# Kernel tuning notes

Measured on AMD Instinct MI355X. Metric: run time of the kernel, lower is better.

## Reference

```python
import jax, jax.numpy as jnp
import numpy as np

I3 = jnp.eye(3, dtype=jnp.float32)
G_VEC = jnp.array([0.0, 0.0, -9.80665], dtype=jnp.float32)
# Q diag: [cov_omega x3, cov_acc x3, cov_b_omega x3, cov_b_acc x3, cov_Rot_c_i x3, cov_t_c_i x3]
Q_DIAG = jnp.array([1e-3] * 3 + [1e-2] * 3 + [6e-9] * 3 + [2e-4] * 3 + [1e-9] * 3 + [1e-9] * 3, dtype=jnp.float32)
N_NORM_ROT = 100
N_NORM_ROT_CI = 1000


def skew(v):
    z = jnp.zeros_like(v[0])
    return jnp.stack([jnp.stack([z, -v[2], v[1]]),
                      jnp.stack([v[2], z, -v[0]]),
                      jnp.stack([-v[1], v[0], z])])


def so3exp(phi):
    a2 = jnp.sum(phi * phi)
    small = a2 < 1e-12
    a = jnp.sqrt(jnp.where(small, 1.0, a2))
    axis = phi / a
    c, s = jnp.cos(a), jnp.sin(a)
    big = c * I3 + (1.0 - c) * jnp.outer(axis, axis) + s * skew(axis)
    return jnp.where(small, I3 + skew(phi), big)


def sen3exp(xi):
    # SE_2(3) exponential: xi[:3]=rotation, xi[3:9]=(v, p) parts
    phi = xi[:3]
    a2 = jnp.sum(phi * phi)
    small = a2 < 1e-12
    a = jnp.sqrt(jnp.where(small, 1.0, a2))
    axis = phi / a
    c, s = jnp.cos(a), jnp.sin(a)
    sk = skew(axis)
    R = jnp.where(small, I3 + skew(phi),
                  c * I3 + (1.0 - c) * jnp.outer(axis, axis) + s * sk)
    J = jnp.where(small, I3 + 0.5 * skew(phi),
                  (s / a) * I3 + (1.0 - s / a) * jnp.outer(axis, axis) + ((1.0 - c) / a) * sk)
    x = J @ xi[3:].reshape(2, 3).T  # (3,2): columns are dv, dp
    return R, x


def normalize_rot(R):
    # Polar-factor re-orthonormalization (equivalent to the SVD-based
    # normalize_rot for near-rotation matrices), via Newton-Schulz iteration
    # which is smooth and jit/vjp friendly.
    def body(X, _):
        return 1.5 * X - 0.5 * (X @ X.T @ X), None
    X, _ = jax.lax.scan(body, R, None, length=8)
    return X


def from_rpy(roll, pitch, yaw):
    cr, sr = jnp.cos(roll), jnp.sin(roll)
    cp, sp = jnp.cos(pitch), jnp.sin(pitch)
    cy, sy = jnp.cos(yaw), jnp.sin(yaw)
    one = jnp.ones_like(cr)
    zero = jnp.zeros_like(cr)
    Rx = jnp.stack([jnp.stack([one, zero, zero]), jnp.stack([zero, cr, -sr]), jnp.stack([zero, sr, cr])])
    Ry = jnp.stack([jnp.stack([cp, zero, sp]), jnp.stack([zero, one, zero]), jnp.stack([-sp, zero, cp])])
    Rz = jnp.stack([jnp.stack([cy, -sy, zero]), jnp.stack([sy, cy, zero]), jnp.stack([zero, zero, one])])
    return Rz @ Ry @ Rx


def init_covariance():
    P = jnp.zeros((21, 21), dtype=jnp.float32)
    P = P.at[:2, :2].set(1e-3 * jnp.eye(2))     # cov_Rot0 (no yaw error)
    P = P.at[3:5, 3:5].set(0.1 * jnp.eye(2))    # cov_v0
    P = P.at[9:12, 9:12].set(6e-3 * I3)         # cov_b_omega0
    P = P.at[12:15, 12:15].set(4e-3 * I3)       # cov_b_acc0
    P = P.at[15:18, 15:18].set(1e-6 * I3)       # cov_Rot_c_i0
    P = P.at[18:21, 18:21].set(5e-3 * I3)       # cov_t_c_i0
    return P


def propagate_cov(P, Rot, v, p, dt):
    F = jnp.zeros((21, 21), dtype=P.dtype)
    F = F.at[3:6, :3].set(skew(G_VEC))
    F = F.at[6:9, 3:6].set(I3)
    F = F.at[:3, 9:12].set(-Rot)
    F = F.at[3:6, 9:12].set(-skew(v) @ Rot)
    F = F.at[3:6, 12:15].set(-Rot)
    F = F.at[6:9, 9:12].set(-skew(p) @ Rot)
    G = jnp.zeros((21, 18), dtype=P.dtype)
    G = G.at[:3, :3].set(Rot)
    G = G.at[3:6, 3:6].set(Rot)
    G = G.at[9:12, 6:9].set(I3)
    G = G.at[12:15, 9:12].set(I3)
    G = G.at[15:18, 12:15].set(I3)
    G = G.at[18:21, 15:18].set(I3)
    F = F * dt
    G = G * dt
    F2 = F @ F
    Phi = jnp.eye(21, dtype=P.dtype) + F + 0.5 * F2 + (F2 @ F) / 6.0  # 3rd-order expm
    return Phi @ (P + (G * Q_DIAG[None, :]) @ G.T) @ Phi.T


def _step(carry, xs):
    Rot, v, p, b_om, b_ac, Rci, tci, P = carry
    u_i, dt_i, mcov_i, i = xs
    # ---- propagate ----
    acc = Rot @ (u_i[3:6] - b_ac) + G_VEC
    v_n = v + acc * dt_i
    p_n = p + v * dt_i + 0.5 * acc * dt_i * dt_i
    Rot_n = Rot @ so3exp((u_i[:3] - b_om) * dt_i)
    P_n = propagate_cov(P, Rot, v, p, dt_i)
    # ---- update: zero lateral/vertical body-velocity pseudo-measurement ----
    omega = u_i[:3] - b_om
    Rot_body = Rot_n @ Rci
    v_imu = Rot_n.T @ v_n
    v_body = Rci.T @ v_imu + skew(tci) @ omega
    H = jnp.zeros((2, 21), dtype=P.dtype)
    H = H.at[:, 3:6].set(Rot_body.T[1:])
    H = H.at[:, 15:18].set((Rci.T @ skew(v_imu))[1:])
    H = H.at[:, 9:12].set(skew(tci)[1:])
    H = H.at[:, 18:21].set(-skew(omega)[1:])
    r = -v_body[1:]
    Rm = jnp.diag(mcov_i)
    S = H @ P_n @ H.T + Rm                    # (2,2)
    K = jnp.linalg.solve(S, H @ P_n).T        # K = P H^T S^-1 (P, S symmetric)
    dx = K @ r                                 # (21,)
    dR, dxi = sen3exp(dx[:9])
    Rot_u = dR @ Rot_n
    v_u = dR @ v_n + dxi[:, 0]
    p_u = dR @ p_n + dxi[:, 1]
    b_om_u = b_om + dx[9:12]
    b_ac_u = b_ac + dx[12:15]
    Rci_u = so3exp(dx[15:18]) @ Rci
    tci_u = tci + dx[18:21]
    IKH = jnp.eye(21, dtype=P.dtype) - K @ H
    P_u = IKH @ P_n @ IKH.T + K @ Rm @ K.T    # Joseph form
    P_u = 0.5 * (P_u + P_u.T)
    Rot_u = jnp.where(i % N_NORM_ROT == 0, normalize_rot(Rot_u), Rot_u)
    Rci_u = jnp.where(i % N_NORM_ROT_CI == 0, normalize_rot(Rci_u), Rci_u)
    carry = (Rot_u, v_u, p_u, b_om_u, b_ac_u, Rci_u, tci_u, P_u)
    return carry, (Rot_u, v_u, p_u, b_om_u, b_ac_u, Rci_u, tci_u)


def _forward(t, u, measurements_covs, v_mes, p_mes, ang0, N):
    dt = t[1:N] - t[:N - 1]
    Rot0 = from_rpy(ang0[0], ang0[1], ang0[2])
    z3 = jnp.zeros(3, dtype=u.dtype)
    carry0 = (Rot0, v_mes[0], z3, z3, z3, I3, z3, init_covariance())
    xs = (u[1:N], dt, measurements_covs[1:N], jnp.arange(1, N))
    _, ys = jax.lax.scan(_step, carry0, xs)
    Rot = jnp.concatenate([Rot0[None], ys[0]], axis=0)
    v = jnp.concatenate([v_mes[0][None], ys[1]], axis=0)
    p = jnp.concatenate([z3[None], ys[2]], axis=0)
    b_omega = jnp.concatenate([z3[None], ys[3]], axis=0)
    b_acc = jnp.concatenate([z3[None], ys[4]], axis=0)
    Rot_c_i = jnp.concatenate([I3[None], ys[5]], axis=0)
    t_c_i = jnp.concatenate([z3[None], ys[6]], axis=0)
    return (Rot, v, p, b_omega, b_acc, Rot_c_i, t_c_i)


def setup_inputs() -> dict:
    key = jax.random.key(0)
    N = 20000  # 200 s at 100 Hz IMU
    k0, k1, k2, k3, k4, k5 = jax.random.split(key, 6)
    t = jnp.arange(N, dtype=jnp.float32) * 0.01
    gyro = 0.01 * jax.random.normal(k0, (N, 3), dtype=jnp.float32)
    acc = jnp.array([0.0, 0.0, 9.80665], jnp.float32) + 0.1 * jax.random.normal(k1, (N, 3), dtype=jnp.float32)
    u = jnp.concatenate([gyro, acc], axis=1)
    measurements_covs = 0.1 + jax.random.uniform(k2, (N, 2), dtype=jnp.float32)
    v_mes = jax.random.normal(k3, (N, 3), dtype=jnp.float32)
    p_mes = jax.random.normal(k4, (N, 3), dtype=jnp.float32)
    ang0 = 0.01 * jax.random.normal(k5, (3,), dtype=jnp.float32)
    return dict(t=t, u=u, measurements_covs=measurements_covs, v_mes=v_mes, p_mes=p_mes, ang0=ang0, N=N)


def reference(t, u, measurements_covs, v_mes, p_mes, ang0, N):
    return _forward(t, u, measurements_covs, v_mes, p_mes, ang0, N)
```

## Files before the change

kernel.cpp:

```cpp
#include <hip/hip_runtime.h>

#define GRAV 9.80665f
#define WAVE_SYNC() do { \
    asm volatile("s_waitcnt lgkmcnt(0)" ::: "memory"); \
    __builtin_amdgcn_sched_barrier(0); \
  } while(0)

#define LDP 28

__device__ __forceinline__ float sel3(int r, float a0, float a1, float a2){
  float x = (r==1)? a1 : a0;
  return (r>=2)? a2 : x;
}
__device__ __forceinline__ float RL(float v, int k){
  return __int_as_float(__builtin_amdgcn_readlane(__float_as_int(v), k));
}
__device__ __forceinline__ float pick9(int k, const float* X){
  float s=X[0];
  s=(k==1)?X[1]:s; s=(k==2)?X[2]:s; s=(k==3)?X[3]:s; s=(k==4)?X[4]:s;
  s=(k==5)?X[5]:s; s=(k==6)?X[6]:s; s=(k==7)?X[7]:s; s=(k==8)?X[8]:s;
  return s;
}

__device__ __forceinline__ void mm33(float* __restrict__ O, const float* A, const float* B){
#pragma unroll
  for(int r=0;r<3;++r){
#pragma unroll
    for(int c=0;c<3;++c){
      O[r*3+c] = A[r*3+0]*B[0*3+c] + A[r*3+1]*B[1*3+c] + A[r*3+2]*B[2*3+c];
    }
  }
}

__device__ __forceinline__ void rot_from_t2(float t_, float p0, float p1, float p2, float* R){
  float c_, k1_, k2_;
  if (t_ < 1e-4f){
    c_  = 1.f - t_*(0.5f - t_*((1.f/24.f) - t_*(1.f/720.f)));
    k2_ = 1.f - t_*((1.f/6.f) - t_*((1.f/120.f) - t_*(1.f/5040.f)));
    k1_ = 0.5f - t_*((1.f/24.f) - t_*(1.f/720.f));
  } else {
    float a = sqrtf(t_);
    c_ = __cosf(a);
    float s = __sinf(a);
    k2_ = s/a;
    k1_ = (1.f - c_)/t_;
  }
  R[0]=c_+k1_*p0*p0;      R[1]=k1_*p0*p1-k2_*p2;  R[2]=k1_*p0*p2+k2_*p1;
  R[3]=k1_*p0*p1+k2_*p2;  R[4]=c_+k1_*p1*p1;      R[5]=k1_*p1*p2-k2_*p0;
  R[6]=k1_*p0*p2-k2_*p1;  R[7]=k1_*p1*p2+k2_*p0;  R[8]=c_+k1_*p2*p2;
}

__device__ __forceinline__ void normalize_rot9(float* X){
#pragma unroll 1
  for(int it=0; it<8; ++it){
    float Y[9], Z[9];
#pragma unroll
    for(int r=0;r<3;++r)
#pragma unroll
      for(int c=0;c<3;++c)
        Y[r*3+c] = X[r*3+0]*X[c*3+0] + X[r*3+1]*X[c*3+1] + X[r*3+2]*X[c*3+2];
#pragma unroll
    for(int r=0;r<3;++r)
#pragma unroll
      for(int c=0;c<3;++c)
        Z[r*3+c] = Y[r*3+0]*X[0*3+c] + Y[r*3+1]*X[1*3+c] + Y[r*3+2]*X[2*3+c];
#pragma unroll
    for(int e=0;e<9;++e) X[e] = 1.5f*X[e] - 0.5f*Z[e];
  }
}

__device__ __forceinline__ float pick_state(int l,
    const float* Rt, const float* vv, const float* pp,
    const float* bw, const float* ba, const float* Rc, const float* tc){
  float s = Rt[0];
  s=(l==1)?Rt[1]:s;  s=(l==2)?Rt[2]:s;  s=(l==3)?Rt[3]:s;  s=(l==4)?Rt[4]:s;
  s=(l==5)?Rt[5]:s;  s=(l==6)?Rt[6]:s;  s=(l==7)?Rt[7]:s;  s=(l==8)?Rt[8]:s;
  s=(l==9)?vv[0]:s;  s=(l==10)?vv[1]:s; s=(l==11)?vv[2]:s;
  s=(l==12)?pp[0]:s; s=(l==13)?pp[1]:s; s=(l==14)?pp[2]:s;
  s=(l==15)?bw[0]:s; s=(l==16)?bw[1]:s; s=(l==17)?bw[2]:s;
  s=(l==18)?ba[0]:s; s=(l==19)?ba[1]:s; s=(l==20)?ba[2]:s;
  s=(l==21)?Rc[0]:s; s=(l==22)?Rc[1]:s; s=(l==23)?Rc[2]:s;
  s=(l==24)?Rc[3]:s; s=(l==25)?Rc[4]:s; s=(l==26)?Rc[5]:s;
  s=(l==27)?Rc[6]:s; s=(l==28)?Rc[7]:s; s=(l==29)?Rc[8]:s;
  s=(l==30)?tc[0]:s; s=(l==31)?tc[1]:s; s=(l==32)?tc[2]:s;
  return s;
}

__global__ __launch_bounds__(64,1)
void iekf_scan_kernel(const float* __restrict__ t,
                      const float* __restrict__ u,
                      const float* __restrict__ mcov,
                      const float* __restrict__ v_mes,
                      const float* __restrict__ ang0,
                      float* __restrict__ out, int N)
{
  const int l = threadIdx.x;
  __shared__ __align__(16) float Pm[21*LDP];
  __shared__ __align__(16) float Eb[21*LDP];

  for (int e=l; e<21*LDP; e+=64){
    int r=e/LDP, c=e-(e/LDP)*LDP;
    float vI=0.f;
    if (r==c){
      if (r<2) vI=0.001f;
      else if (r==3||r==4) vI=0.1f;
      else if (r>=9&&r<12) vI=0.006f;
      else if (r>=12&&r<15) vI=0.004f;
      else if (r>=15&&r<18) vI=1e-6f;
      else if (r>=18&&r<21) vI=0.005f;
    }
    Pm[e]=vI;
  }

  int ostr=0; float* op = out;
  {
    int obase=0, ooff=0;
    if (l<9)       {obase=0;    ostr=9; ooff=l;}
    else if (l<12) {obase=9*N;  ostr=3; ooff=l-9;}
    else if (l<15) {obase=12*N; ostr=3; ooff=l-12;}
    else if (l<18) {obase=15*N; ostr=3; ooff=l-15;}
    else if (l<21) {obase=18*N; ostr=3; ooff=l-18;}
    else if (l<30) {obase=21*N; ostr=9; ooff=l-21;}
    else           {obase=30*N; ostr=3; ooff=l-30;}
    op = out + obase + ooff;
  }

  const int g21 = l/21;
  const int c21 = l - g21*21;
  const int cw  = 9 + 4*g21;
  int l1 = l+21; if (l1>=63) l1-=63;
  int l2 = l+42; if (l2>=63) l2-=63;
  static const int cols[12] = {3,4,5, 9,10,11, 15,16,17, 18,19,20};

  float myval = 0.f;
  {
    float Rt0[9], vv0[3], pp0[3], bwa[3], baa[3], Rc0[9], tca[3];
    float rl = ang0[0], pt = ang0[1], yw = ang0[2];
    float cr=cosf(rl), sr=sinf(rl), cp=cosf(pt), sp=sinf(pt), cy=cosf(yw), sy=sinf(yw);
    Rt0[0]=cy*cp; Rt0[1]=cy*sp*sr - sy*cr; Rt0[2]=cy*sp*cr + sy*sr;
    Rt0[3]=sy*cp; Rt0[4]=sy*sp*sr + cy*cr; Rt0[5]=sy*sp*cr - cy*sr;
    Rt0[6]=-sp;   Rt0[7]=cp*sr;            Rt0[8]=cp*cr;
    vv0[0]=v_mes[0]; vv0[1]=v_mes[1]; vv0[2]=v_mes[2];
#pragma unroll
    for(int k=0;k<3;++k){ pp0[k]=0.f; bwa[k]=0.f; baa[k]=0.f; tca[k]=0.f; }
    Rc0[0]=1.f;Rc0[1]=0.f;Rc0[2]=0.f;Rc0[3]=0.f;Rc0[4]=1.f;Rc0[5]=0.f;Rc0[6]=0.f;Rc0[7]=0.f;Rc0[8]=1.f;
    float sv = pick_state(l, Rt0, vv0, pp0, bwa, baa, Rc0, tca);
    if (l<33){ op[0] = sv; myval = sv; }
  }
  WAVE_SYNC();

  float tA = t[0], tB = t[1];
  float cu[6];
#pragma unroll
  for(int k=0;k<6;++k) cu[k]=u[6+k];
  float cm0=mcov[2], cm1=mcov[3];

  int nx100=100, nx1000=1000;

#pragma unroll 1
  for (int i=1; i<N; ++i){
    float dt = tB - tA;
    float u0=cu[0], u1=cu[1], u2=cu[2], u3=cu[3], u4=cu[4], u5=cu[5];
    float crm0=cm0, crm1=cm1;
    if (i+1 < N){
      tA = tB; tB = t[i+1];
#pragma unroll
      for(int k=0;k<6;++k) cu[k]=u[(i+1)*6+k];
      cm0 = mcov[(i+1)*2]; cm1 = mcov[(i+1)*2+1];
    }

    float Rt[9];
#pragma unroll
    for(int k=0;k<9;++k) Rt[k] = RL(myval, k);
    float vv0s=RL(myval,9),  vv1s=RL(myval,10), vv2s=RL(myval,11);
    float pp0s=RL(myval,12), pp1s=RL(myval,13), pp2s=RL(myval,14);
    float bw0=RL(myval,15),  bw1=RL(myval,16),  bw2=RL(myval,17);
    float ba0=RL(myval,18),  ba1=RL(myval,19),  ba2=RL(myval,20);
    float Rc[9];
#pragma unroll
    for(int k=0;k<9;++k) Rc[k] = RL(myval, 21+k);
    float tc0=RL(myval,30), tc1=RL(myval,31), tc2=RL(myval,32);

    float dt2=dt*dt, gdt=GRAV*dt, hdt=0.5f*dt, hdt2=0.5f*dt*dt;
    float hgdt2 = 0.5f*gdt*dt;
    float g6d   = gdt*dt2*(1.0f/6.0f);

    float w0=u0-bw0, w1=u1-bw1, w2=u2-bw2;
    float aa0=u3-ba0, aa1=u4-ba1, aa2=u5-ba2;
    float acc0 = Rt[0]*aa0+Rt[1]*aa1+Rt[2]*aa2;
    float acc1 = Rt[3]*aa0+Rt[4]*aa1+Rt[5]*aa2;
    float acc2 = Rt[6]*aa0+Rt[7]*aa1+Rt[8]*aa2 - GRAV;
    float vn0=vv0s+acc0*dt, vn1=vv1s+acc1*dt, vn2=vv2s+acc2*dt;
    float pn0=pp0s+vv0s*dt+acc0*hdt2;
    float pn1=pp1s+vv1s*dt+acc1*hdt2;
    float pn2=pp2s+vv2s*dt+acc2*hdt2;
    float ph0=w0*dt, ph1=w1*dt, ph2=w2*dt;
    float dRs[9]; rot_from_t2(ph0*ph0+ph1*ph1+ph2*ph2, ph0,ph1,ph2, dRs);
    float Rn[9]; mm33(Rn, Rt, dRs);

    float RtG[3], RtA[3], RtB[3];
#pragma unroll
    for(int k=0;k<3;++k){
      float r0=Rt[k], r3=Rt[3+k], r6=Rt[6+k];
      RtG[k] = sel3(g21, r0, r3, r6);
      RtA[k] = sel3(g21, r3, r6, r0);
      RtB[k] = sel3(g21, r6, r0, r3);
    }
    float vAs = sel3(g21, vv2s, vv0s, vv1s), vBs = sel3(g21, vv1s, vv2s, vv0s);
    float pAs = sel3(g21, pp2s, pp0s, pp1s), pBs = sel3(g21, pp1s, pp2s, pp0s);
    float Bs0,Bs1,Bs2, Cs0,Cs1,Cs2, Ds0,Ds1,Ds2;
    {
      float bs[3], cs[3], ds[3];
#pragma unroll
      for(int k=0;k<3;++k){
        bs[k] = -dt*RtG[k];
        float craw = dt*(vAs*RtA[k] - vBs*RtB[k]);
        float selC = sel3(g21, -RtA[k], RtB[k], 0.f);
        cs[k] = craw + hgdt2*selC;
        float draw = dt*(pAs*RtA[k] - pBs*RtB[k]);
        ds[k] = draw + hdt*craw + g6d*selC;
      }
      Bs0=bs[0];Bs1=bs[1];Bs2=bs[2];
      Cs0=cs[0];Cs1=cs[1];Cs2=cs[2];
      Ds0=ds[0];Ds1=ds[1];Ds2=ds[2];
    }

    float q0d=0.001f*dt2, q1d=0.01f*dt2;
    float q69=6e-9f*dt2, q24=2e-4f*dt2, q19=1e-9f*dt2;

    if (l<63){
      int c = c21;
      const float4* Pr4 = (const float4*)(Pm + c*LDP);
      float4 a0=Pr4[0], a1=Pr4[1], a2=Pr4[2], a3=Pr4[3], a4=Pr4[4];
      float m20 = Pm[c*LDP + 20];

      bool cl3 = (c<3);
      bool c36 = (c>=3 && c<6);
      int csel = c36 ? (c-3) : (cl3 ? c : 0);
      float Rtc0 = sel3(csel, Rt[0], Rt[3], Rt[6]);
      float Rtc1 = sel3(csel, Rt[1], Rt[4], Rt[7]);
      float Rtc2 = sel3(csel, Rt[2], Rt[5], Rt[8]);
      float dot0 = Rt[0]*Rtc0 + Rt[1]*Rtc1 + Rt[2]*Rtc2;
      float dot1 = Rt[3]*Rtc0 + Rt[4]*Rtc1 + Rt[5]*Rtc2;
      float dotg = RtG[0]*Rtc0 + RtG[1]*Rtc1 + RtG[2]*Rtc2;

      float m0  = a0.x + (cl3 ? q0d*dot0 : 0.f);
      float m1  = a0.y + (cl3 ? q0d*dot1 : 0.f);
      float mr  = sel3(g21, a0.x, a0.y, a0.z) + (cl3 ? q0d*dotg : 0.f);
      float m3r = sel3(g21, a0.w, a1.x, a1.y) + (c36 ? q1d*dotg : 0.f);
      float m6r = sel3(g21, a1.z, a1.w, a2.x);
      float m9  = a2.y + ((c==9) ? q69 : 0.f);
      float m10 = a2.z + ((c==10)? q69 : 0.f);
      float m11 = a2.w + ((c==11)? q69 : 0.f);
      float m12 = a3.x + ((c==12)? q24 : 0.f);
      float m13 = a3.y + ((c==13)? q24 : 0.f);
      float m14 = a3.z + ((c==14)? q24 : 0.f);

      float Ar = (g21==0)? gdt*m1 : (g21==1)? -gdt*m0 : 0.f;
      float bterm = Bs0*m12+Bs1*m13+Bs2*m14;
      float e0 = mr + Bs0*m9+Bs1*m10+Bs2*m11;
      float e1 = m3r + Ar + Cs0*m9+Cs1*m10+Cs2*m11 + bterm;
      float e2 = m6r + hdt*Ar + dt*m3r + Ds0*m9+Ds1*m10+Ds2*m11 + hdt*bterm;
      Eb[g21*LDP+c]=e0; Eb[(3+g21)*LDP+c]=e1; Eb[(6+g21)*LDP+c]=e2;

      float mc0 = sel3(g21, a2.y, a3.y, a4.y);
      float mc1 = sel3(g21, a2.z, a3.z, a4.z);
      float mc2 = sel3(g21, a2.w, a3.w, a4.w);
      float mc3 = sel3(g21, a3.x, a4.x, m20);
      float qd0 = sel3(g21, q69, q24, q19);
      float qd1 = sel3(g21, q69, q24, q19);
      float qd2 = sel3(g21, q69, q19, q19);
      float qd3 = sel3(g21, q24, q19, q19);
      Eb[(cw+0)*LDP+c] = mc0 + ((cw+0==c)? qd0 : 0.f);
      Eb[(cw+1)*LDP+c] = mc1 + ((cw+1==c)? qd1 : 0.f);
      Eb[(cw+2)*LDP+c] = mc2 + ((cw+2==c)? qd2 : 0.f);
      Eb[(cw+3)*LDP+c] = mc3 + ((cw+3==c)? qd3 : 0.f);
    }

    float H0[12], H1[12];
    float rr0, rr1;
    {
      float Rb1 = Rn[0]*Rc[1]+Rn[1]*Rc[4]+Rn[2]*Rc[7];
      float Rb4 = Rn[3]*Rc[1]+Rn[4]*Rc[4]+Rn[5]*Rc[7];
      float Rb7 = Rn[6]*Rc[1]+Rn[7]*Rc[4]+Rn[8]*Rc[7];
      float Rb2 = Rn[0]*Rc[2]+Rn[1]*Rc[5]+Rn[2]*Rc[8];
      float Rb5 = Rn[3]*Rc[2]+Rn[4]*Rc[5]+Rn[5]*Rc[8];
      float Rb8 = Rn[6]*Rc[2]+Rn[7]*Rc[5]+Rn[8]*Rc[8];
      float vi0 = Rn[0]*vn0+Rn[3]*vn1+Rn[6]*vn2;
      float vi1 = Rn[1]*vn0+Rn[4]*vn1+Rn[7]*vn2;
      float vi2 = Rn[2]*vn0+Rn[5]*vn1+Rn[8]*vn2;
      float vb1 = Rc[1]*vi0+Rc[4]*vi1+Rc[7]*vi2 + (tc2*w0 - tc0*w2);
      float vb2 = Rc[2]*vi0+Rc[5]*vi1+Rc[8]*vi2 + (tc0*w1 - tc1*w0);
      rr0 = -vb1; rr1 = -vb2;
      H0[0]=Rb1; H0[1]=Rb4; H0[2]=Rb7;
      H1[0]=Rb2; H1[1]=Rb5; H1[2]=Rb8;
      H0[3]=tc2;  H0[4]=0.f;  H0[5]=-tc0;
      H1[3]=-tc1; H1[4]=tc0;  H1[5]=0.f;
      H0[6]=Rc[4]*vi2 - Rc[7]*vi1;  H0[7]=Rc[7]*vi0 - Rc[1]*vi2;  H0[8]=Rc[1]*vi1 - Rc[4]*vi0;
      H1[6]=Rc[5]*vi2 - Rc[8]*vi1;  H1[7]=Rc[8]*vi0 - Rc[2]*vi2;  H1[8]=Rc[2]*vi1 - Rc[5]*vi0;
      H0[9]=-w2; H0[10]=0.f; H0[11]=w0;
      H1[9]=w1;  H1[10]=-w0; H1[11]=0.f;
    }
    WAVE_SYNC();

    float pnv[7];
#pragma unroll
    for(int k=0;k<7;++k) pnv[k]=0.f;
    float p0=0.f, p1=0.f;
    if (l<63){
      int r = c21;
      const float4* Er4 = (const float4*)(Eb + r*LDP);
      float4 a0=Er4[0], a1=Er4[1], a2=Er4[2], a3=Er4[3], a4=Er4[4];
      float e20 = Eb[r*LDP + 20];

      float e0a=a0.x, e1a=a0.y;
      float eg  = sel3(g21, a0.x, a0.y, a0.z);
      float e3g = sel3(g21, a0.w, a1.x, a1.y);
      float e6g = sel3(g21, a1.z, a1.w, a2.x);
      float e9=a2.y, e10=a2.z, e11=a2.w, e12=a3.x, e13=a3.y, e14=a3.z;

      float Ag = (g21==0)? gdt*e1a : (g21==1)? -gdt*e0a : 0.f;
      float bterm = Bs0*e12+Bs1*e13+Bs2*e14;
      pnv[0] = eg + Bs0*e9+Bs1*e10+Bs2*e11;
      pnv[1] = e3g + Ag + Cs0*e9+Cs1*e10+Cs2*e11 + bterm;
      pnv[2] = e6g + hdt*Ag + dt*e3g + Ds0*e9+Ds1*e10+Ds2*e11 + hdt*bterm;
      pnv[3] = sel3(g21, a2.y, a3.y, a4.y);
      pnv[4] = sel3(g21, a2.z, a3.z, a4.z);
      pnv[5] = sel3(g21, a2.w, a3.w, a4.w);
      pnv[6] = sel3(g21, a3.x, a4.x, e20);

      float c1a = sel3(g21, H0[0], H0[1], H0[2]);
      float c3a = sel3(g21, H0[3], 0.f,   H0[8]);
      float c4a = sel3(g21, H0[4], 0.f,   H0[9]);
      float c5a = sel3(g21, H0[5], H0[6], H0[10]);
      float c6a = sel3(g21, 0.f,   H0[7], H0[11]);
      float c1b = sel3(g21, H1[0], H1[1], H1[2]);
      float c3b = sel3(g21, H1[3], 0.f,   H1[8]);
      float c4b = sel3(g21, H1[4], 0.f,   H1[9]);
      float c5b = sel3(g21, H1[5], H1[6], H1[10]);
      float c6b = sel3(g21, 0.f,   H1[7], H1[11]);
      p0 = c1a*pnv[1] + c3a*pnv[3] + c4a*pnv[4] + c5a*pnv[5] + c6a*pnv[6];
      p1 = c1b*pnv[1] + c3b*pnv[3] + c4b*pnv[4] + c5b*pnv[5] + c6b*pnv[6];
    }
    float hpr0 = p0 + __shfl(p0, l1) + __shfl(p0, l2);
    float hpr1 = p1 + __shfl(p1, l1) + __shfl(p1, l2);

    float hpjx[7], hpjy[7];
#pragma unroll
    for (int s=0;s<7;++s){
      int j = (s<3)? (g21 + 3*s) : (cw + (s-3));
      hpjx[s] = __shfl(hpr0, j);
      hpjy[s] = __shfl(hpr1, j);
    }

    float hph00=0.f, hph01=0.f, hph10=0.f, hph11=0.f;
#pragma unroll
    for(int k=0;k<12;++k){
      float hp0 = RL(hpr0, cols[k]);
      float hp1 = RL(hpr1, cols[k]);
      hph00 += hp0*H0[k]; hph01 += hp0*H1[k];
      hph10 += hp1*H0[k]; hph11 += hp1*H1[k];
    }
    float s00 = hph00 + crm0, s01 = hph01, s10 = hph10, s11 = hph11 + crm1;
    float idet = 1.0f/(s00*s11 - s01*s10);
    float i00 =  s11*idet, i01 = -s01*idet, i10 = -s10*idet, i11 = s00*idet;
    float K0 = i00*hpr0 + i01*hpr1;
    float K1 = i10*hpr0 + i11*hpr1;
    float s01q = 0.5f*(s01 + s10);
    float dxval = K0*rr0 + K1*rr1;

    float dx0 = RL(dxval,0), dx1 = RL(dxval,1), dx2 = RL(dxval,2);
    float dx3 = RL(dxval,3), dx4 = RL(dxval,4), dx5 = RL(dxval,5);
    float dx6 = RL(dxval,6), dx7 = RL(dxval,7), dx8 = RL(dxval,8);
    float dx15 = RL(dxval,15), dx16 = RL(dxval,16), dx17 = RL(dxval,17);
    int src = (l>=30 && l<33)? (l-12) : ((l>=15 && l<21)? (l-6) : 0);
    float dxadd = __shfl(dxval, src);

    if (l<63){
      int r = c21;
#pragma unroll
      for (int s=0;s<7;++s){
        int j = (s<3)? (g21 + 3*s) : (cw + (s-3));
        float kjx = i00*hpjx[s] + i01*hpjy[s];
        float kjy = i10*hpjx[s] + i11*hpjy[s];
        float cross = (K0*hpjx[s] + K1*hpjy[s]) + (kjx*hpr0 + kjy*hpr1);
        float quad  = (K0*kjx)*s00 + (K0*kjy + K1*kjx)*s01q + (K1*kjy)*s11;
        float val = pnv[s] - cross + quad;
        if (r <= j){
          Pm[r*LDP+j] = val;
          if (r < j) Pm[j*LDP+r] = val;
        }
      }
    }

    float t2x = dx0*dx0+dx1*dx1+dx2*dx2;
    float cX,k1X,k2X,j1X;
    if (t2x < 1e-4f){
      cX  = 1.f - t2x*(0.5f - t2x*((1.f/24.f) - t2x*(1.f/720.f)));
      k2X = 1.f - t2x*((1.f/6.f) - t2x*((1.f/120.f) - t2x*(1.f/5040.f)));
      k1X = 0.5f - t2x*((1.f/24.f) - t2x*(1.f/720.f));
      j1X = (1.f/6.f) - t2x*((1.f/120.f) - t2x*(1.f/5040.f));
    } else {
      float a = sqrtf(t2x);
      cX = __cosf(a);
      float s = __sinf(a);
      k2X = s/a; k1X = (1.f-cX)/t2x; j1X = (1.f-k2X)/t2x;
    }
    float dR[9];
    dR[0]=cX+k1X*dx0*dx0;      dR[1]=k1X*dx0*dx1-k2X*dx2; dR[2]=k1X*dx0*dx2+k2X*dx1;
    dR[3]=k1X*dx0*dx1+k2X*dx2; dR[4]=cX+k1X*dx1*dx1;      dR[5]=k1X*dx1*dx2-k2X*dx0;
    dR[6]=k1X*dx0*dx2-k2X*dx1; dR[7]=k1X*dx1*dx2+k2X*dx0; dR[8]=cX+k1X*dx2*dx2;
    float Jm[9];
    Jm[0]=k2X+j1X*dx0*dx0;      Jm[1]=j1X*dx0*dx1-k1X*dx2; Jm[2]=j1X*dx0*dx2+k1X*dx1;
    Jm[3]=j1X*dx0*dx1+k1X*dx2;  Jm[4]=k2X+j1X*dx1*dx1;     Jm[5]=j1X*dx1*dx2-k1X*dx0;
    Jm[6]=j1X*dx0*dx2-k1X*dx1;  Jm[7]=j1X*dx1*dx2+k1X*dx0; Jm[8]=k2X+j1X*dx2*dx2;
    float Ec[9];
    rot_from_t2(dx15*dx15+dx16*dx16+dx17*dx17, dx15,dx16,dx17, Ec);

    float nv = 0.f;
    if (l<9){
      int ro=(l>=6)?2:((l>=3)?1:0); int co=l-3*ro;
      float d0=sel3(ro,dR[0],dR[3],dR[6]), d1=sel3(ro,dR[1],dR[4],dR[7]), d2=sel3(ro,dR[2],dR[5],dR[8]);
      float n0=sel3(co,Rn[0],Rn[1],Rn[2]), n1=sel3(co,Rn[3],Rn[4],Rn[5]), n2=sel3(co,Rn[6],Rn[7],Rn[8]);
      nv = d0*n0 + d1*n1 + d2*n2;
    } else if (l<15){
      int j=l-9; bool isv=(j<3); int ro = isv? j : (j-3);
      float x0 = isv? vn0:pn0, x1 = isv? vn1:pn1, x2 = isv? vn2:pn2;
      float y0 = isv? dx3:dx6, y1 = isv? dx4:dx7, y2 = isv? dx5:dx8;
      float d0=sel3(ro,dR[0],dR[3],dR[6]), d1=sel3(ro,dR[1],dR[4],dR[7]), d2=sel3(ro,dR[2],dR[5],dR[8]);
      float j0=sel3(ro,Jm[0],Jm[3],Jm[6]), j1m=sel3(ro,Jm[1],Jm[4],Jm[7]), j2m=sel3(ro,Jm[2],Jm[5],Jm[8]);
      nv = d0*x0 + d1*x1 + d2*x2 + j0*y0 + j1m*y1 + j2m*y2;
    } else if (l<21){
      float old = (l<18)? sel3(l-15,bw0,bw1,bw2) : sel3(l-18,ba0,ba1,ba2);
      nv = old + dxadd;
    } else if (l<30){
      int j=l-21; int ro=(j>=6)?2:((j>=3)?1:0); int co=j-3*ro;
      float e0=sel3(ro,Ec[0],Ec[3],Ec[6]), e1=sel3(ro,Ec[1],Ec[4],Ec[7]), e2=sel3(ro,Ec[2],Ec[5],Ec[8]);
      float r0=sel3(co,Rc[0],Rc[1],Rc[2]), r1=sel3(co,Rc[3],Rc[4],Rc[5]), r2=sel3(co,Rc[6],Rc[7],Rc[8]);
      nv = e0*r0 + e1*r1 + e2*r2;
    } else if (l<33){
      nv = sel3(l-30,tc0,tc1,tc2) + dxadd;
    }
    if (l<33) myval = nv;

    bool n100 = (i==nx100), n1000 = (i==nx1000);
    if (n100) nx100 += 100;
    if (n1000) nx1000 += 1000;
    if (n100 || n1000){
      if (n100){
        float X[9];
#pragma unroll
        for (int k=0;k<9;++k) X[k]=RL(myval,k);
        normalize_rot9(X);
        if (l<9) myval = pick9(l,X);
      }
      if (n1000){
        float Y[9];
#pragma unroll
        for (int k=0;k<9;++k) Y[k]=RL(myval,21+k);
        normalize_rot9(Y);
        if (l>=21 && l<30) myval = pick9(l-21,Y);
      }
    }

    if (l<33) op[i*ostr] = myval;

    WAVE_SYNC();
  }
}

extern "C" void kernel_launch(void* const* d_in, const int* in_sizes, int n_in,
                              void* d_out, int out_size, void* d_ws, size_t ws_size,
                              hipStream_t stream) {
  (void)n_in; (void)out_size; (void)d_ws; (void)ws_size;
  const float* t     = (const float*)d_in[0];
  const float* u     = (const float*)d_in[1];
  const float* mcov  = (const float*)d_in[2];
  const float* v_mes = (const float*)d_in[3];
  const float* ang0  = (const float*)d_in[5];
  int N = in_sizes[0];
  iekf_scan_kernel<<<dim3(1), dim3(64), 0, stream>>>(t, u, mcov, v_mes, ang0, (float*)d_out, N);
}
```

Measured before the change: 49.86 ms.

## Broadcast state via LDS, hoist covariance propagation, symmetrize P update through shared

Replaces 33 per-step readlane broadcasts of the filter state with vectorized LDS float4 reads from a shared state buffer. The covariance propagation block is moved ahead of the state propagation to shorten the dependency chain. The Joseph-form covariance update now stages predicted P and HP in shared memory and writes a symmetrized average, replacing the shuffle-based gather and conditional mirror writes. This adds an extra wave sync per step and changes numerics slightly by averaging the two triangles.

```diff
diff --git a/kernel.cpp b/kernel.cpp
--- a/kernel.cpp
+++ b/kernel.cpp
@@ -97,6 +97,9 @@
   const int l = threadIdx.x;
   __shared__ __align__(16) float Pm[21*LDP];
   __shared__ __align__(16) float Eb[21*LDP];
+  __shared__ __align__(16) float PnS[21*LDP];
+  __shared__ float2 HPs2[21];
+  __shared__ __align__(16) float stS[36];
 
   for (int e=l; e<21*LDP; e+=64){
     int r=e/LDP, c=e-(e/LDP)*LDP;
@@ -132,7 +135,6 @@
   int l2 = l+42; if (l2>=63) l2-=63;
   static const int cols[12] = {3,4,5, 9,10,11, 15,16,17, 18,19,20};
 
-  float myval = 0.f;
   {
     float Rt0[9], vv0[3], pp0[3], bwa[3], baa[3], Rc0[9], tca[3];
     float rl = ang0[0], pt = ang0[1], yw = ang0[2];
@@ -145,7 +147,8 @@
     for(int k=0;k<3;++k){ pp0[k]=0.f; bwa[k]=0.f; baa[k]=0.f; tca[k]=0.f; }
     Rc0[0]=1.f;Rc0[1]=0.f;Rc0[2]=0.f;Rc0[3]=0.f;Rc0[4]=1.f;Rc0[5]=0.f;Rc0[6]=0.f;Rc0[7]=0.f;Rc0[8]=1.f;
     float sv = pick_state(l, Rt0, vv0, pp0, bwa, baa, Rc0, tca);
-    if (l<33){ op[0] = sv; myval = sv; }
+    if (l<33){ op[0] = sv; stS[l] = sv; }
+    if (l>=33 && l<36) stS[l] = 0.f;
   }
   WAVE_SYNC();
 
@@ -169,21 +172,98 @@
       cm0 = mcov[(i+1)*2]; cm1 = mcov[(i+1)*2+1];
     }
 
-    float Rt[9];
-#pragma unroll
-    for(int k=0;k<9;++k) Rt[k] = RL(myval, k);
-    float vv0s=RL(myval,9),  vv1s=RL(myval,10), vv2s=RL(myval,11);
-    float pp0s=RL(myval,12), pp1s=RL(myval,13), pp2s=RL(myval,14);
-    float bw0=RL(myval,15),  bw1=RL(myval,16),  bw2=RL(myval,17);
-    float ba0=RL(myval,18),  ba1=RL(myval,19),  ba2=RL(myval,20);
-    float Rc[9];
-#pragma unroll
-    for(int k=0;k<9;++k) Rc[k] = RL(myval, 21+k);
-    float tc0=RL(myval,30), tc1=RL(myval,31), tc2=RL(myval,32);
+    const float4* st4 = (const float4*)stS;
+    float4 q0=st4[0], q1=st4[1], q2=st4[2], q3=st4[3], q4=st4[4], q5=st4[5], q6=st4[6], q7=st4[7], q8=st4[8];
+    float Rt[9] = {q0.x,q0.y,q0.z,q0.w,q1.x,q1.y,q1.z,q1.w,q2.x};
+    float vv0s=q2.y, vv1s=q2.z, vv2s=q2.w;
+    float pp0s=q3.x, pp1s=q3.y, pp2s=q3.z;
+    float bw0=q3.w, bw1=q4.x, bw2=q4.y;
+    float ba0=q4.z, ba1=q4.w, ba2=q5.x;
+    float Rc[9] = {q5.y,q5.z,q5.w,q6.x,q6.y,q6.z,q6.w,q7.x,q7.y};
+    float tc0=q7.z, tc1=q7.w, tc2=q8.x;
 
     float dt2=dt*dt, gdt=GRAV*dt, hdt=0.5f*dt, hdt2=0.5f*dt*dt;
     float hgdt2 = 0.5f*gdt*dt;
     float g6d   = gdt*dt2*(1.0f/6.0f);
+
+    float RtG[3], RtA[3], RtB[3];
+#pragma unroll
+    for(int k=0;k<3;++k){
+      float r0=Rt[k], r3=Rt[3+k], r6=Rt[6+k];
+      RtG[k] = sel3(g21, r0, r3, r6);
+      RtA[k] = sel3(g21, r3, r6, r0);
+      RtB[k] = sel3(g21, r6, r0, r3);
+    }
+    float vAs = sel3(g21, vv2s, vv0s, vv1s), vBs = sel3(g21, vv1s, vv2s, vv0s);
+    float pAs = sel3(g21, pp2s, pp0s, pp1s), pBs = sel3(g21, pp1s, pp2s, pp0s);
+    float Bs0,Bs1,Bs2, Cs0,Cs1,Cs2, Ds0,Ds1,Ds2;
+    {
+      float bs[3], cs[3], ds[3];
+#pragma unroll
+      for(int k=0;k<3;++k){
+        bs[k] = -dt*RtG[k];
+        float craw = dt*(vAs*RtA[k] - vBs*RtB[k]);
+        float selC = sel3(g21, -RtA[k], RtB[k], 0.f);
+        cs[k] = craw + hgdt2*selC;
+        float draw = dt*(pAs*RtA[k] - pBs*RtB[k]);
+        ds[k] = draw + hdt*craw + g6d*selC;
+      }
+      Bs0=bs[0];Bs1=bs[1];Bs2=bs[2];
+      Cs0=cs[0];Cs1=cs[1];Cs2=cs[2];
+      Ds0=ds[0];Ds1=ds[1];Ds2=ds[2];
+    }
+
+    float q0d=0.001f*dt2, q1d=0.01f*dt2;
+    float q69=6e-9f*dt2, q24=2e-4f*dt2, q19=1e-9f*dt2;
+
+    if (l<63){
+      int c = c21;
+      const float4* Pr4 = (const float4*)(Pm + c*LDP);
+      float4 a0=Pr4[0], a1=Pr4[1], a2=Pr4[2], a3=Pr4[3], a4=Pr4[4];
+      float m20 = Pm[c*LDP + 20];
+
+      bool cl3 = (c<3);
+      bool c36 = (c>=3 && c<6);
+      int csel = c36 ? (c-3) : (cl3 ? c : 0);
+      float Rtc0 = sel3(csel, Rt[0], Rt[3], Rt[6]);
+      float Rtc1 = sel3(csel, Rt[1], Rt[4], Rt[7]);
+      float Rtc2 = sel3(csel, Rt[2], Rt[5], Rt[8]);
+      float dot0 = Rt[0]*Rtc0 + Rt[1]*Rtc1 + Rt[2]*Rtc2;
+      float dot1 = Rt[3]*Rtc0 + Rt[4]*Rtc1 + Rt[5]*Rtc2;
+      float dotg = RtG[0]*Rtc0 + RtG[1]*Rtc1 + RtG[2]*Rtc2;
+
+      float m0  = a0.x + (cl3 ? q0d*dot0 : 0.f);
+      float m1  = a0.y + (cl3 ? q0d*dot1 : 0.f);
+      float mr  = sel3(g21, a0.x, a0.y, a0.z) + (cl3 ? q0d*dotg : 0.f);
+      float m3r = sel3(g21, a0.w, a1.x, a1.y) + (c36 ? q1d*dotg : 0.f);
+      float m6r = sel3(g21, a1.z, a1.w, a2.x);
+      float m9  = a2.y + ((c==9) ? q69 : 0.f);
+      float m10 = a2.z + ((c==10)? q69 : 0.f);
+      float m11 = a2.w + ((c==11)? q69 : 0.f);
+      float m12 = a3.x + ((c==12)? q24 : 0.f);
+      float m13 = a3.y + ((c==13)? q24 : 0.f);
+      float m14 = a3.z + ((c==14)? q24 : 0.f);
+
+      float Ar = (g21==0)? gdt*m1 : (g21==1)? -gdt*m0 : 0.f;
+      float bterm = Bs0*m12+Bs1*m13+Bs2*m14;
+      float e0 = mr + Bs0*m9+Bs1*m10+Bs2*m11;
+      float e1 = m3r + Ar + Cs0*m9+Cs1*m10+Cs2*m11 + bterm;
+      float e2 = m6r + hdt*Ar + dt*m3r + Ds0*m9+Ds1*m10+Ds2*m11 + hdt*bterm;
+      Eb[g21*LDP+c]=e0; Eb[(3+g21)*LDP+c]=e1; Eb[(6+g21)*LDP+c]=e2;
+
+      float mc0 = sel3(g21, a2.y, a3.y, a4.y);
+      float mc1 = sel3(g21, a2.z, a3.z, a4.z);
+      float mc2 = sel3(g21, a2.w, a3.w, a4.w);
+      float mc3 = sel3(g21, a3.x, a4.x, m20);
+      float qd0 = sel3(g21, q69, q24, q19);
+      float qd1 = sel3(g21, q69, q24, q19);
+      float qd2 = sel3(g21, q69, q19, q19);
+      float qd3 = sel3(g21, q24, q19, q19);
+      Eb[(cw+0)*LDP+c] = mc0 + ((cw+0==c)? qd0 : 0.f);
+      Eb[(cw+1)*LDP+c] = mc1 + ((cw+1==c)? qd1 : 0.f);
+      Eb[(cw+2)*LDP+c] = mc2 + ((cw+2==c)? qd2 : 0.f);
+      Eb[(cw+3)*LDP+c] = mc3 + ((cw+3==c)? qd3 : 0.f);
+    }
 
     float w0=u0-bw0, w1=u1-bw1, w2=u2-bw2;
     float aa0=u3-ba0, aa1=u4-ba1, aa2=u5-ba2;
@@ -197,85 +277,6 @@
     float ph0=w0*dt, ph1=w1*dt, ph2=w2*dt;
     float dRs[9]; rot_from_t2(ph0*ph0+ph1*ph1+ph2*ph2, ph0,ph1,ph2, dRs);
     float Rn[9]; mm33(Rn, Rt, dRs);
-
-    float RtG[3], RtA[3], RtB[3];
-#pragma unroll
-    for(int k=0;k<3;++k){
-      float r0=Rt[k], r3=Rt[3+k], r6=Rt[6+k];
-      RtG[k] = sel3(g21, r0, r3, r6);
-      RtA[k] = sel3(g21, r3, r6, r0);
-      RtB[k] = sel3(g21, r6, r0, r3);
-    }
-    float vAs = sel3(g21, vv2s, vv0s, vv1s), vBs = sel3(g21, vv1s, vv2s, vv0s);
-    float pAs = sel3(g21, pp2s, pp0s, pp1s), pBs = sel3(g21, pp1s, pp2s, pp0s);
-    float Bs0,Bs1,Bs2, Cs0,Cs1,Cs2, Ds0,Ds1,Ds2;
-    {
-      float bs[3], cs[3], ds[3];
-#pragma unroll
-      for(int k=0;k<3;++k){
-        bs[k] = -dt*RtG[k];
-        float craw = dt*(vAs*RtA[k] - vBs*RtB[k]);
-        float selC = sel3(g21, -RtA[k], RtB[k], 0.f);
-        cs[k] = craw + hgdt2*selC;
-        float draw = dt*(pAs*RtA[k] - pBs*RtB[k]);
-        ds[k] = draw + hdt*craw + g6d*selC;
-      }
-      Bs0=bs[0];Bs1=bs[1];Bs2=bs[2];
-      Cs0=cs[0];Cs1=cs[1];Cs2=cs[2];
-      Ds0=ds[0];Ds1=ds[1];Ds2=ds[2];
-    }
-
-    float q0d=0.001f*dt2, q1d=0.01f*dt2;
-    float q69=6e-9f*dt2, q24=2e-4f*dt2, q19=1e-9f*dt2;
-
-    if (l<63){
-      int c = c21;
-      const float4* Pr4 = (const float4*)(Pm + c*LDP);
-      float4 a0=Pr4[0], a1=Pr4[1], a2=Pr4[2], a3=Pr4[3], a4=Pr4[4];
-      float m20 = Pm[c*LDP + 20];
-
-      bool cl3 = (c<3);
-      bool c36 = (c>=3 && c<6);
-      int csel = c36 ? (c-3) : (cl3 ? c : 0);
-      float Rtc0 = sel3(csel, Rt[0], Rt[3], Rt[6]);
-      float Rtc1 = sel3(csel, Rt[1], Rt[4], Rt[7]);
-      float Rtc2 = sel3(csel, Rt[2], Rt[5], Rt[8]);
-      float dot0 = Rt[0]*Rtc0 + Rt[1]*Rtc1 + Rt[2]*Rtc2;
-      float dot1 = Rt[3]*Rtc0 + Rt[4]*Rtc1 + Rt[5]*Rtc2;
-      float dotg = RtG[0]*Rtc0 + RtG[1]*Rtc1 + RtG[2]*Rtc2;
-
-      float m0  = a0.x + (cl3 ? q0d*dot0 : 0.f);
-      float m1  = a0.y + (cl3 ? q0d*dot1 : 0.f);
-      float mr  = sel3(g21, a0.x, a0.y, a0.z) + (cl3 ? q0d*dotg : 0.f);
-      float m3r = sel3(g21, a0.w, a1.x, a1.y) + (c36 ? q1d*dotg : 0.f);
-      float m6r = sel3(g21, a1.z, a1.w, a2.x);
-      float m9  = a2.y + ((c==9) ? q69 : 0.f);
-      float m10 = a2.z + ((c==10)? q69 : 0.f);
-      float m11 = a2.w + ((c==11)? q69 : 0.f);
-      float m12 = a3.x + ((c==12)? q24 : 0.f);
-      float m13 = a3.y + ((c==13)? q24 : 0.f);
-      float m14 = a3.z + ((c==14)? q24 : 0.f);
-
-      float Ar = (g21==0)? gdt*m1 : (g21==1)? -gdt*m0 : 0.f;
-      float bterm = Bs0*m12+Bs1*m13+Bs2*m14;
-      float e0 = mr + Bs0*m9+Bs1*m10+Bs2*m11;
-      float e1 = m3r + Ar + Cs0*m9+Cs1*m10+Cs2*m11 + bterm;
-      float e2 = m6r + hdt*Ar + dt*m3r + Ds0*m9+Ds1*m10+Ds2*m11 + hdt*bterm;
-      Eb[g21*LDP+c]=e0; Eb[(3+g21)*LDP+c]=e1; Eb[(6+g21)*LDP+c]=e2;
-
-      float mc0 = sel3(g21, a2.y, a3.y, a4.y);
-      float mc1 = sel3(g21, a2.z, a3.z, a4.z);
-      float mc2 = sel3(g21, a2.w, a3.w, a4.w);
-      float mc3 = sel3(g21, a3.x, a4.x, m20);
-      float qd0 = sel3(g21, q69, q24, q19);
-      float qd1 = sel3(g21, q69, q24, q19);
-      float qd2 = sel3(g21, q69, q19, q19);
-      float qd3 = sel3(g21, q24, q19, q19);
-      Eb[(cw+0)*LDP+c] = mc0 + ((cw+0==c)? qd0 : 0.f);
-      Eb[(cw+1)*LDP+c] = mc1 + ((cw+1==c)? qd1 : 0.f);
-      Eb[(cw+2)*LDP+c] = mc2 + ((cw+2==c)? qd2 : 0.f);
-      Eb[(cw+3)*LDP+c] = mc3 + ((cw+3==c)? qd3 : 0.f);
-    }
 
     float H0[12], H1[12];
     float rr0, rr1;
@@ -329,6 +330,14 @@
       pnv[5] = sel3(g21, a2.w, a3.w, a4.w);
       pnv[6] = sel3(g21, a3.x, a4.x, e20);
 
+      PnS[r*LDP + g21]   = pnv[0];
+      PnS[r*LDP + 3+g21] = pnv[1];
+      PnS[r*LDP + 6+g21] = pnv[2];
+      PnS[r*LDP + cw]    = pnv[3];
+      PnS[r*LDP + cw+1]  = pnv[4];
+      PnS[r*LDP + cw+2]  = pnv[5];
+      PnS[r*LDP + cw+3]  = pnv[6];
+
       float c1a = sel3(g21, H0[0], H0[1], H0[2]);
       float c3a = sel3(g21, H0[3], 0.f,   H0[8]);
       float c4a = sel3(g21, H0[4], 0.f,   H0[9]);
@@ -344,14 +353,7 @@
     }
     float hpr0 = p0 + __shfl(p0, l1) + __shfl(p0, l2);
     float hpr1 = p1 + __shfl(p1, l1) + __shfl(p1, l2);
-
-    float hpjx[7], hpjy[7];
-#pragma unroll
-    for (int s=0;s<7;++s){
-      int j = (s<3)? (g21 + 3*s) : (cw + (s-3));
-      hpjx[s] = __shfl(hpr0, j);
-      hpjy[s] = __shfl(hpr1, j);
-    }
+    if (l<21) HPs2[l] = make_float2(hpr0, hpr1);
 
     float hph00=0.f, hph01=0.f, hph10=0.f, hph11=0.f;
 #pragma unroll
@@ -375,23 +377,6 @@
     float dx15 = RL(dxval,15), dx16 = RL(dxval,16), dx17 = RL(dxval,17);
     int src = (l>=30 && l<33)? (l-12) : ((l>=15 && l<21)? (l-6) : 0);
     float dxadd = __shfl(dxval, src);
-
-    if (l<63){
-      int r = c21;
-#pragma unroll
-      for (int s=0;s<7;++s){
-        int j = (s<3)? (g21 + 3*s) : (cw + (s-3));
-        float kjx = i00*hpjx[s] + i01*hpjy[s];
-        float kjy = i10*hpjx[s] + i11*hpjy[s];
-        float cross = (K0*hpjx[s] + K1*hpjy[s]) + (kjx*hpr0 + kjy*hpr1);
-        float quad  = (K0*kjx)*s00 + (K0*kjy + K1*kjx)*s01q + (K1*kjy)*s11;
-        float val = pnv[s] - cross + quad;
-        if (r <= j){
-          Pm[r*LDP+j] = val;
-          if (r < j) Pm[j*LDP+r] = val;
-        }
-      }
-    }
 
     float t2x = dx0*dx0+dx1*dx1+dx2*dx2;
     float cX,k1X,k2X,j1X;
@@ -417,49 +402,68 @@
     float Ec[9];
     rot_from_t2(dx15*dx15+dx16*dx16+dx17*dx17, dx15,dx16,dx17, Ec);
 
-    float nv = 0.f;
+    WAVE_SYNC();
+
+    if (l<63){
+      int r = c21;
+#pragma unroll
+      for (int s=0;s<7;++s){
+        int j = (s<3)? (g21 + 3*s) : (cw + (s-3));
+        float pnT = PnS[j*LDP + r];
+        float2 hpj = HPs2[j];
+        float kjx = i00*hpj.x + i01*hpj.y;
+        float kjy = i10*hpj.x + i11*hpj.y;
+        float base  = 0.5f*(pnv[s] + pnT);
+        float cross = (K0*hpj.x + K1*hpj.y) + (kjx*hpr0 + kjy*hpr1);
+        float quad  = (K0*kjx)*s00 + (K0*kjy + K1*kjx)*s01q + (K1*kjy)*s11;
+        Pm[r*LDP+j] = base - cross + quad;
+      }
+    }
+
+    float myval = 0.f;
     if (l<9){
       int ro=(l>=6)?2:((l>=3)?1:0); int co=l-3*ro;
       float d0=sel3(ro,dR[0],dR[3],dR[6]), d1=sel3(ro,dR[1],dR[4],dR[7]), d2=sel3(ro,dR[2],dR[5],dR[8]);
       float n0=sel3(co,Rn[0],Rn[1],Rn[2]), n1=sel3(co,Rn[3],Rn[4],Rn[5]), n2=sel3(co,Rn[6],Rn[7],Rn[8]);
-      nv = d0*n0 + d1*n1 + d2*n2;
+      myval = d0*n0 + d1*n1 + d2*n2;
     } else if (l<15){
       int j=l-9; bool isv=(j<3); int ro = isv? j : (j-3);
       float x0 = isv? vn0:pn0, x1 = isv? vn1:pn1, x2 = isv? vn2:pn2;
       float y0 = isv? dx3:dx6, y1 = isv? dx4:dx7, y2 = isv? dx5:dx8;
       float d0=sel3(ro,dR[0],dR[3],dR[6]), d1=sel3(ro,dR[1],dR[4],dR[7]), d2=sel3(ro,dR[2],dR[5],dR[8]);
       float j0=sel3(ro,Jm[0],Jm[3],Jm[6]), j1m=sel3(ro,Jm[1],Jm[4],Jm[7]), j2m=sel3(ro,Jm[2],Jm[5],Jm[8]);
-      nv = d0*x0 + d1*x1 + d2*x2 + j0*y0 + j1m*y1 + j2m*y2;
+      myval = d0*x0 + d1*x1 + d2*x2 + j0*y0 + j1m*y1 + j2m*y2;
     } else if (l<21){
       float old = (l<18)? sel3(l-15,bw0,bw1,bw2) : sel3(l-18,ba0,ba1,ba2);
-      nv = old + dxadd;
+      myval = old + dxadd;
     } else if (l<30){
       int j=l-21; int ro=(j>=6)?2:((j>=3)?1:0); int co=j-3*ro;
       float e0=sel3(ro,Ec[0],Ec[3],Ec[6]), e1=sel3(ro,Ec[1],Ec[4],Ec[7]), e2=sel3(ro,Ec[2],Ec[5],Ec[8]);
       float r0=sel3(co,Rc[0],Rc[1],Rc[2]), r1=sel3(co,Rc[3],Rc[4],Rc[5]), r2=sel3(co,Rc[6],Rc[7],Rc[8]);
-      nv = e0*r0 + e1*r1 + e2*r2;
+      myval = e0*r0 + e1*r1 + e2*r2;
     } else if (l<33){
-      nv = sel3(l-30,tc0,tc1,tc2) + dxadd;
-    }
-    if (l<33) myval = nv;
+      myval = sel3(l-30,tc0,tc1,tc2) + dxadd;
+    }
+    if (l<33) stS[l] = myval;
 
     bool n100 = (i==nx100), n1000 = (i==nx1000);
     if (n100) nx100 += 100;
     if (n1000) nx1000 += 1000;
     if (n100 || n1000){
+      WAVE_SYNC();
       if (n100){
         float X[9];
 #pragma unroll
-        for (int k=0;k<9;++k) X[k]=RL(myval,k);
+        for (int k=0;k<9;++k) X[k]=stS[k];
         normalize_rot9(X);
-        if (l<9) myval = pick9(l,X);
+        if (l<9){ myval = pick9(l,X); stS[l] = myval; }
       }
       if (n1000){
         float Y[9];
 #pragma unroll
-        for (int k=0;k<9;++k) Y[k]=RL(myval,21+k);
+        for (int k=0;k<9;++k) Y[k]=stS[21+k];
         normalize_rot9(Y);
-        if (l>=21 && l<30) myval = pick9(l-21,Y);
+        if (l>=21 && l<30){ myval = pick9(l-21,Y); stS[l] = myval; }
       }
     }
 
```

Result: faster. 44.25 ms (-11.3%).
